# Performance work log

Measured on AMD Instinct MI355X. Metric: run time of the kernel, lower is better.

The kernel has to match this reference:

```python
import jax, jax.numpy as jnp
from jax import lax
import numpy as np

D_MODEL = 384; D_INNER = 768; D_STATE = 16; D_CONV = 4; DT_RANK = 24
BATCH = 2; SEQ = 4096


def _mamba(x, in_w, conv_w, conv_b, xproj_w, dt_w, dt_b, A_log, Dp, out_w):
    # x: [B, L, D_MODEL]
    xz = x @ in_w.T                                   # [B, L, 2*D_INNER]
    xi, z = jnp.split(xz, 2, axis=-1)
    xc = jnp.swapaxes(xi, 1, 2)                       # [B, D_INNER, L]
    xc = lax.conv_general_dilated(xc, conv_w, (1,), [(D_CONV - 1, 0)],
                                  feature_group_count=D_INNER)  # causal depthwise conv
    xc = jax.nn.silu(xc + conv_b[None, :, None])
    xc = jnp.swapaxes(xc, 1, 2)                       # [B, L, D_INNER]
    xdbl = xc @ xproj_w.T                             # [B, L, DT_RANK + 2*D_STATE]
    dt = xdbl[..., :DT_RANK]
    Bm = xdbl[..., DT_RANK:DT_RANK + D_STATE]
    Cm = xdbl[..., DT_RANK + D_STATE:]
    delta = jax.nn.softplus(dt @ dt_w.T + dt_b)       # [B, L, D_INNER]
    A = -jnp.exp(A_log)                               # [D_INNER, D_STATE]

    def step(h, inp):
        d_t, x_t, B_t, C_t = inp                      # [B,Di],[B,Di],[B,N],[B,N]
        dA = jnp.exp(d_t[..., None] * A)              # [B, Di, N]
        h = dA * h + (d_t * x_t)[..., None] * B_t[:, None, :]
        return h, jnp.einsum('bdn,bn->bd', h, C_t)

    xs = tuple(jnp.swapaxes(a, 0, 1) for a in (delta, xc, Bm, Cm))  # time-major
    h0 = jnp.zeros((x.shape[0], D_INNER, D_STATE), x.dtype)
    _, ys = lax.scan(step, h0, xs)                    # ys: [L, B, D_INNER]
    y = jnp.swapaxes(ys, 0, 1) + xc * Dp              # skip term D*x
    return (y * jax.nn.silu(z)) @ out_w.T             # [B, L, D_MODEL]


def _forward(x, fp, bp, c_w, c_b, gn_w, gn_b):
    xt = jnp.swapaxes(x, 1, 2)                        # [B, L, C]
    yf = _mamba(xt, *fp)
    yb = _mamba(xt[:, ::-1, :], *bp)                  # note: source does NOT flip back
    y = jnp.concatenate([yf, yb], axis=2)             # [B, L, 2C]
    y = jnp.swapaxes(y, 1, 2)                         # [B, 2C, L]
    y = jnp.einsum('oc,bcl->bol', c_w[:, :, 0], y) + c_b[None, :, None]  # 1x1 conv
    a, b = jnp.split(y, 2, axis=1)                    # GLU over channel dim
    y = a * jax.nn.sigmoid(b)                         # [B, C, L]
    mu = y.mean(axis=(1, 2), keepdims=True)           # GroupNorm(1, C)
    var = y.var(axis=(1, 2), keepdims=True)
    y = (y - mu) / jnp.sqrt(var + 1e-5)
    return y * gn_w[None, :, None] + gn_b[None, :, None]


def setup_inputs() -> dict:
    key = jax.random.key(0)
    it = iter(jax.random.split(key, 20))

    def nrm(shape, s=0.02):
        return jax.random.normal(next(it), shape, jnp.float32) * s

    def mamba_params(pref):
        return {
            pref + 'in_w': nrm((2 * D_INNER, D_MODEL)),
            pref + 'conv_w': nrm((D_INNER, 1, D_CONV), 0.3),
            pref + 'conv_b': nrm((D_INNER,)),
            pref + 'xproj_w': nrm((DT_RANK + 2 * D_STATE, D_INNER)),
            pref + 'dt_w': nrm((D_INNER, DT_RANK), 0.1),
            pref + 'dt_b': nrm((D_INNER,)),
            pref + 'A_log': jnp.log(jnp.tile(jnp.arange(1.0, D_STATE + 1.0, dtype=jnp.float32), (D_INNER, 1))),
            pref + 'D': jnp.ones((D_INNER,), jnp.float32),
            pref + 'out_w': nrm((D_MODEL, D_INNER)),
        }

    inp = {'x': jax.random.normal(next(it), (BATCH, D_MODEL, SEQ), jnp.float32)}
    inp.update(mamba_params('f_'))
    inp.update(mamba_params('b_'))
    inp['c_w'] = nrm((2 * D_MODEL, 2 * D_MODEL, 1))
    inp['c_b'] = nrm((2 * D_MODEL,))
    inp['gn_w'] = jnp.ones((D_MODEL,), jnp.float32)
    inp['gn_b'] = jnp.zeros((D_MODEL,), jnp.float32)
    return inp


def reference(x, f_in_w, f_conv_w, f_conv_b, f_xproj_w, f_dt_w, f_dt_b, f_A_log, f_D, f_out_w,
              b_in_w, b_conv_w, b_conv_b, b_xproj_w, b_dt_w, b_dt_b, b_A_log, b_D, b_out_w,
              c_w, c_b, gn_w, gn_b):
    fp = (f_in_w, f_conv_w, f_conv_b, f_xproj_w, f_dt_w, f_dt_b, f_A_log, f_D, f_out_w)
    bp = (b_in_w, b_conv_w, b_conv_b, b_xproj_w, b_dt_w, b_dt_b, b_A_log, b_D, b_out_w)
    return _forward(x, fp, bp, c_w, c_b, gn_w, gn_b)
```

## Files before the change

kernel.cpp:

```cpp
#include <hip/hip_runtime.h>
#include <hip/hip_bf16.h>
#include <hip/hip_fp16.h>

typedef unsigned short u16;
typedef unsigned int   u32;
typedef __bf16  bf16x8 __attribute__((ext_vector_type(8)));
typedef float   f32x4  __attribute__((ext_vector_type(4)));

#define BL   8192
#define LSEQ 4096
#define DI   768
#define CHUNK 32
#define NCHUNK (LSEQ / CHUNK)
#define CTC  16
#define LOG2E 1.44269504088896340736f

#define LOAD_LDS16(g, l) __builtin_amdgcn_global_load_lds( \
    (const __attribute__((address_space(1))) void*)(g), \
    (__attribute__((address_space(3))) void*)(l), 16, 0, 0)

static __device__ __forceinline__ float bf2f(u16 u) {
    union { float f; u32 i; } v; v.i = ((u32)u) << 16; return v.f;
}
static __device__ __forceinline__ u16 f2bs(float f) {
    union { float f; u32 i; } v; v.f = f;
    u32 r = v.i + 0x7fffu + ((v.i >> 16) & 1u);
    return (u16)(r >> 16);
}
static __device__ __forceinline__ float ldf(const void* p, size_t i, int f32) {
    return f32 ? ((const float*)p)[i] : bf2f(((const u16*)p)[i]);
}

__global__ void detect_dtype(const void* __restrict__ gnw, int* __restrict__ flag) {
    u32 bits = *(const u32*)gnw;
    *flag = ((bits & 0xFFFFu) == 0u) ? 1 : 0;
}

__global__ void check_apow(const void* __restrict__ a_f, const void* __restrict__ a_b,
                           int* __restrict__ apow, const int* __restrict__ flag) {
    int f = *flag;
    __shared__ int ok;
    if (threadIdx.x == 0) ok = 1;
    __syncthreads();
    for (int i = threadIdx.x; i < 2 * 12288; i += 256) {
        const void* a = (i >= 12288) ? a_b : a_f;
        int idx = i % 12288;
        int d = idx >> 4, n = idx & 15;
        float An = __expf(ldf(a, idx, f));
        float rf = __expf(ldf(a, d * 16, f)) * (float)(n + 1);
        if (fabsf(An - rf) > 1e-5f * fabsf(rf)) ok = 0;
    }
    __syncthreads();
    if (threadIdx.x == 0) *apow = ok;
}

__global__ void cvt_bf16_3(const void* __restrict__ s0, const void* __restrict__ s1,
                           const void* __restrict__ s2, u16* __restrict__ dst,
                           int n0, int n1, int ntot, const int* __restrict__ flag) {
    int i = blockIdx.x * 256 + threadIdx.x;
    if (i >= ntot) return;
    int f = *flag;
    const void* s; size_t off;
    if (i < n0)      { s = s0; off = i; }
    else if (i < n1) { s = s1; off = i - n0; }
    else             { s = s2; off = i - n1; }
    dst[i] = f ? f2bs(((const float*)s)[off]) : ((const u16*)s)[off];
}

__global__ void cvt_conv(const void* __restrict__ cw_f, const void* __restrict__ cw_b,
                         const void* __restrict__ cb_f, const void* __restrict__ cb_b,
                         float* __restrict__ cwf, float* __restrict__ cbf,
                         const int* __restrict__ flag) {
    int i = blockIdx.x * 256 + threadIdx.x;
    int f = *flag;
    if (i < 2 * 3072)
        cwf[i] = ldf(i < 3072 ? cw_f : cw_b, i % 3072, f);
    int j = i - 2 * 3072;
    if (j >= 0 && j < 2 * 768)
        cbf[j] = ldf(j < 768 ? cb_f : cb_b, j % 768, f);
}

__global__ void transpose_x(const void* __restrict__ x, u16* __restrict__ xT,
                            const int* __restrict__ flag) {
    __shared__ u16 tile[32][33];
    int f = *flag;
    int b  = blockIdx.z;
    int l0 = blockIdx.x * 32, c0 = blockIdx.y * 32;
    int li = threadIdx.x, ci = threadIdx.y;
    for (int cc = ci; cc < 32; cc += 8) {
        size_t idx = (size_t)(b * 384 + c0 + cc) * LSEQ + l0 + li;
        tile[cc][li] = f ? f2bs(((const float*)x)[idx]) : ((const u16*)x)[idx];
    }
    __syncthreads();
    for (int lc = ci; lc < 32; lc += 8)
        xT[(size_t)(b * LSEQ + l0 + lc) * 384 + c0 + li] = tile[li][lc];
}

__global__ void transpose_ow(const void* __restrict__ ow_f, const void* __restrict__ ow_b,
                             u16* __restrict__ owT, const int* __restrict__ flag) {
    __shared__ u16 tile[32][33];
    int f = *flag;
    int dir = blockIdx.z;
    const void* ow = dir ? ow_b : ow_f;
    int c0 = blockIdx.x * 32, d0 = blockIdx.y * 32;
    int di = threadIdx.x, ci = threadIdx.y;
    for (int cc = ci; cc < 32; cc += 8) {
        size_t idx = (size_t)(c0 + cc) * 768 + d0 + di;
        tile[cc][di] = f ? f2bs(((const float*)ow)[idx]) : ((const u16*)ow)[idx];
    }
    __syncthreads();
    for (int dd = ci; dd < 32; dd += 8)
        owT[(size_t)dir * 294912 + (size_t)(d0 + dd) * 384 + c0 + di] = tile[di][dd];
}

__global__ void build_wcomb(const void* __restrict__ xp_f, const void* __restrict__ dtw_f,
                            const void* __restrict__ xp_b, const void* __restrict__ dtw_b,
                            u16* __restrict__ Wc, const int* __restrict__ flag) {
    int f = *flag;
    int dir = blockIdx.y;
    const void* xp  = dir ? xp_b  : xp_f;
    const void* dtw = dir ? dtw_b : dtw_f;
    u16* W = Wc + (size_t)dir * 896 * 768;
    int idx = blockIdx.x * 256 + threadIdx.x;
    if (idx >= 896 * 768) return;
    int nrow = idx / 768, k = idx - nrow * 768;
    float v = 0.f;
    if (nrow < 768) {
#pragma unroll
        for (int r = 0; r < 24; r++)
            v = fmaf(ldf(dtw, nrow * 24 + r, f), ldf(xp, r * 768 + k, f), v);
    } else if (nrow < 800) {
        v = ldf(xp, (24 + (nrow - 768)) * 768 + k, f);
    }
    W[idx] = f2bs(v);
}

__global__ __launch_bounds__(256) void gemm_mfma(
    const u16* __restrict__ A, int lda, size_t aStr,
    const u16* __restrict__ W, int ldw, size_t wStr,
    int K, int MB, int NB, int Nstore, int mode,
    u16* __restrict__ ob0, u16* __restrict__ ob1,
    float* __restrict__ of0, float* __restrict__ of1,
    const void* __restrict__ bias0, const void* __restrict__ bias1,
    const int* __restrict__ flag) {
    __shared__ __align__(16) u16 lA[2][128 * 32];
    __shared__ __align__(16) u16 lB[2][128 * 32];
    const int f = *flag;
    const int tid = threadIdx.x;
    const int wave = tid >> 6, lane = tid & 63;
    const int flat = blockIdx.x;
    const int mb = flat % MB;
    const int rest = flat / MB;
    const int nb = rest % NB;
    const int dir = rest / NB;
    const int m0 = mb * 128, n0 = nb * 128;
    const int wr = (wave >> 1) * 64, wc = (wave & 1) * 64;
    const int fr = lane & 15, fq = lane >> 4;
    const void* bias = dir ? bias1 : bias0;

    f32x4 acc[4][4];
#pragma unroll
    for (int i = 0; i < 4; i++)
#pragma unroll
        for (int j = 0; j < 4; j++) acc[i][j] = 0.f;

    const int srow = wave * 16 + (lane >> 2);
    const int scol = (lane & 3) * 8;
    const u16* gA0 = A + (size_t)dir * aStr + (size_t)(m0 + srow) * lda + scol;
    const u16* gA1 = gA0 + (size_t)64 * lda;
    const u16* gB0 = W + (size_t)dir * wStr + (size_t)(n0 + srow) * ldw + scol;
    const u16* gB1 = gB0 + (size_t)64 * ldw;

    LOAD_LDS16(gA0, &lA[0][wave * 512]);
    LOAD_LDS16(gA1, &lA[0][2048 + wave * 512]);
    LOAD_LDS16(gB0, &lB[0][wave * 512]);
    LOAD_LDS16(gB1, &lB[0][2048 + wave * 512]);

    int cur = 0;
    for (int k0 = 0; k0 < K; k0 += 32) {
        __syncthreads();
        if (k0 + 32 < K) {
            gA0 += 32; gA1 += 32; gB0 += 32; gB1 += 32;
            int nx = cur ^ 1;
            LOAD_LDS16(gA0, &lA[nx][wave * 512]);
            LOAD_LDS16(gA1, &lA[nx][2048 + wave * 512]);
            LOAD_LDS16(gB0, &lB[nx][wave * 512]);
            LOAD_LDS16(gB1, &lB[nx][2048 + wave * 512]);
        }
        bf16x8 af[4], bfr[4];
#pragma unroll
        for (int i = 0; i < 4; i++) af[i]  = *(const bf16x8*)&lA[cur][(wr + i * 16 + fr) * 32 + fq * 8];
#pragma unroll
        for (int j = 0; j < 4; j++) bfr[j] = *(const bf16x8*)&lB[cur][(wc + j * 16 + fr) * 32 + fq * 8];
#pragma unroll
        for (int i = 0; i < 4; i++)
#pragma unroll
            for (int j = 0; j < 4; j++)
                acc[i][j] = __builtin_amdgcn_mfma_f32_16x16x32_bf16(af[i], bfr[j], acc[i][j], 0, 0, 0);
        cur ^= 1;
    }

    const int lr = (lane >> 4) * 4, lc = lane & 15;
#pragma unroll
    for (int i = 0; i < 4; i++) {
#pragma unroll
        for (int j = 0; j < 4; j++) {
#pragma unroll
            for (int rg = 0; rg < 4; rg++) {
                int m = m0 + wr + i * 16 + lr + rg;
                int n = n0 + wc + j * 16 + lc;
                if (n >= Nstore) continue;
                float v = acc[i][j][rg];
                if (mode == 0) {
                    int bI = m >> 12, l = m & 4095;
                    size_t r = dir ? ((size_t)bI * LSEQ + (LSEQ - 1 - l)) : (size_t)m;
                    if (n < 768) ob0[(size_t)dir * BL * DI + r * 768 + n] = f2bs(v);
                    else         ob1[(size_t)dir * BL * DI + r * 768 + (n - 768)] = f2bs(v);
                } else if (mode == 1) {
                    if (n < 768) {
                        float xp = v + ldf(bias, n, f);
                        float sp = fmaxf(xp, 0.f) + __logf(1.f + __expf(-fabsf(xp)));
                        ((__half*)ob0)[(size_t)dir * BL * DI + (size_t)m * 768 + n] = __float2half_rn(sp);
                    } else {
                        of1[(size_t)dir * BL * 32 + (size_t)m * 32 + (n - 768)] = v;
                    }
                } else if (mode == 2) {
                    ob0[(size_t)m * 1536 + dir * 768 + n] = f2bs(v);
                } else {
                    of0[(size_t)m * 768 + n] = v + ldf(bias, n, f);
                }
            }
        }
    }
}

__global__ __launch_bounds__(256) void conv_silu(
    const u16* __restrict__ xi, u16* __restrict__ xc,
    const float* __restrict__ cwf, const float* __restrict__ cbf) {
    int gid = blockIdx.x * 256 + threadIdx.x;
    int dg = gid % 96;
    int rest = gid / 96;
    int tc = rest % (LSEQ / CTC);
    int bd = rest / (LSEQ / CTC);
    int dir = bd >> 1;
    int d0 = dg * 8;
    float w[32], bias[8];
#pragma unroll
    for (int q = 0; q < 8; q++) *(float4*)&w[q * 4] = *(const float4*)&cwf[dir * 3072 + d0 * 4 + q * 4];
    *(float4*)&bias[0] = *(const float4*)&cbf[dir * 768 + d0];
    *(float4*)&bias[4] = *(const float4*)&cbf[dir * 768 + d0 + 4];
    size_t rowbase = (size_t)bd * LSEQ;
    int t0 = tc * CTC;
    uint4 zero; zero.x = zero.y = zero.z = zero.w = 0u;
    uint4 win[4];
#pragma unroll
    for (int i = 0; i < 3; i++) {
        int tt = t0 - 3 + i;
        win[i] = (tt >= 0) ? *(const uint4*)&xi[(rowbase + tt) * DI + d0] : zero;
    }
    uint4 nxt = *(const uint4*)&xi[(rowbase + t0) * DI + d0];
#pragma unroll 4
    for (int i = 0; i < CTC; i++) {
        win[3] = nxt;
        if (i + 1 < CTC) nxt = *(const uint4*)&xi[(rowbase + t0 + i + 1) * DI + d0];
        float acc[8];
#pragma unroll
        for (int c = 0; c < 8; c++) acc[c] = bias[c];
#pragma unroll
        for (int tap = 0; tap < 4; tap++) {
            const u16* pv = (const u16*)&win[tap];
#pragma unroll
            for (int c = 0; c < 8; c++)
                acc[c] = fmaf(w[c * 4 + tap], bf2f(pv[c]), acc[c]);
        }
        u16 ov[8];
#pragma unroll
        for (int c = 0; c < 8; c++) ov[c] = f2bs(acc[c] / (1.f + __expf(-acc[c])));
        *(uint4*)&xc[(rowbase + t0 + i) * DI + d0] = *(const uint4*)ov;
        win[0] = win[1]; win[1] = win[2]; win[2] = win[3];
    }
}

__global__ __launch_bounds__(256) void scan_phase1(
    const __half* __restrict__ delta, const u16* __restrict__ xc,
    const float* __restrict__ bc,
    __half* __restrict__ S, __half* __restrict__ sumdl,
    const void* __restrict__ alog_f, const void* __restrict__ alog_b,
    const int* __restrict__ flag, const int* __restrict__ apow) {
    int f = *flag, ap = *apow;
    int dblk = blockIdx.x, chunk = blockIdx.y, bd = blockIdx.z;
    int dir = bd >> 1;
    const void* alog = dir ? alog_b : alog_f;
    int d = dblk * 256 + threadIdx.x;
    size_t rowbase = (size_t)bd * LSEQ;
    float h[16];
#pragma unroll
    for (int n = 0; n < 16; n++) h[n] = 0.f;
    float An2_0 = -__expf(ldf(alog, d * 16, f)) * LOG2E;
    int t0 = chunk * CHUNK;
    size_t off = (rowbase + t0) * DI + d;
    const float* bcG = bc + (rowbase + t0) * 32;
    float sd = 0.f;
    if (ap) {
#pragma unroll 2
        for (int i = 0; i < CHUNK; i++, off += DI) {
            float Bv[16];
#pragma unroll
            for (int q = 0; q < 4; q++) *(float4*)&Bv[q * 4] = *(const float4*)&bcG[(size_t)i * 32 + q * 4];
            float dl = __half2float(delta[off]);
            float u = dl * bf2f(xc[off]);
            sd += dl;
            float e[16];
            float e1 = exp2f(dl * An2_0);
            e[0]=e1; e[1]=e1*e1; e[2]=e[1]*e1; e[3]=e[1]*e[1];
            e[4]=e[3]*e[0]; e[5]=e[3]*e[1]; e[6]=e[3]*e[2]; e[7]=e[3]*e[3];
            e[8]=e[7]*e[0]; e[9]=e[7]*e[1]; e[10]=e[7]*e[2]; e[11]=e[7]*e[3];
            e[12]=e[7]*e[4]; e[13]=e[7]*e[5]; e[14]=e[7]*e[6]; e[15]=e[7]*e[7];
#pragma unroll
            for (int n = 0; n < 16; n++) h[n] = fmaf(e[n], h[n], u * Bv[n]);
        }
    } else {
        float An2[16];
#pragma unroll
        for (int n = 0; n < 16; n++) An2[n] = -__expf(ldf(alog, d * 16 + n, f)) * LOG2E;
#pragma unroll 2
        for (int i = 0; i < CHUNK; i++, off += DI) {
            float Bv[16];
#pragma unroll
            for (int q = 0; q < 4; q++) *(float4*)&Bv[q * 4] = *(const float4*)&bcG[(size_t)i * 32 + q * 4];
            float dl = __half2float(delta[off]);
            float u = dl * bf2f(xc[off]);
            sd += dl;
#pragma unroll
            for (int n = 0; n < 16; n++)
                h[n] = fmaf(exp2f(dl * An2[n]), h[n], u * Bv[n]);
        }
    }
    __half hs[16];
#pragma unroll
    for (int n = 0; n < 16; n++) hs[n] = __float2half(h[n]);
    __half* Sp = S + (((size_t)bd * NCHUNK + chunk) * 768 + d) * 16;
    *(uint4*)&Sp[0] = *(const uint4*)&hs[0];
    *(uint4*)&Sp[8] = *(const uint4*)&hs[8];
    sumdl[((size_t)bd * NCHUNK + chunk) * 768 + d] = __float2half(sd);
}

__global__ __launch_bounds__(256) void scan_fixup(
    __half* __restrict__ S, const __half* __restrict__ sumdl,
    const void* __restrict__ alog_f, const void* __restrict__ alog_b,
    const int* __restrict__ flag) {
    int f = *flag;
    int gid = blockIdx.x * 256 + threadIdx.x;
    int bd = gid / 12288;
    int r  = gid % 12288;
    int d = r >> 4, n = r & 15;
    const void* alog = (bd >> 1) ? alog_b : alog_f;
    float An2 = -__expf(ldf(alog, d * 16 + n, f)) * LOG2E;
    float h = 0.f;
#pragma unroll 4
    for (int c = 0; c < NCHUNK; c++) {
        size_t sidx = (((size_t)bd * NCHUNK + c) * 768 + d) * 16 + n;
        float s  = __half2float(S[sidx]);
        float sd = __half2float(sumdl[((size_t)bd * NCHUNK + c) * 768 + d]);
        S[sidx] = __float2half(h);
        h = fmaf(exp2f(An2 * sd), h, s);
    }
}

__global__ __launch_bounds__(256) void scan_phase3(
    const __half* __restrict__ delta, const u16* __restrict__ xc,
    const float* __restrict__ bc, const u16* __restrict__ zz,
    const __half* __restrict__ S, u16* __restrict__ ygi,
    const void* __restrict__ alog_f, const void* __restrict__ alog_b,
    const void* __restrict__ D_f, const void* __restrict__ D_b,
    const int* __restrict__ flag, const int* __restrict__ apow) {
    int f = *flag, ap = *apow;
    int dblk = blockIdx.x, chunk = blockIdx.y, bd = blockIdx.z;
    int dir = bd >> 1, b = bd & 1;
    const void* alog = dir ? alog_b : alog_f;
    const void* Dp   = dir ? D_b   : D_f;
    int d = dblk * 256 + threadIdx.x;
    size_t rowbase = (size_t)bd * LSEQ;
    float An2_0 = -__expf(ldf(alog, d * 16, f)) * LOG2E;
    float h[16];
    {
        const __half* Sp = S + (((size_t)bd * NCHUNK + chunk) * 768 + d) * 16;
        uint4 sv0 = *(const uint4*)&Sp[0];
        uint4 sv1 = *(const uint4*)&Sp[8];
        const __half* ph0 = (const __half*)&sv0;
        const __half* ph1 = (const __half*)&sv1;
#pragma unroll
        for (int n = 0; n < 8; n++) { h[n] = __half2float(ph0[n]); h[n + 8] = __half2float(ph1[n]); }
    }
    float Dd = ldf(Dp, d, f);
    int t0 = chunk * CHUNK;
    size_t off = (rowbase + t0) * DI + d;
    size_t oidx = ((size_t)b * LSEQ + t0) * 1536 + dir * 768 + d;
    const float* bcG = bc + (rowbase + t0) * 32;
    if (ap) {
#pragma unroll 2
        for (int i = 0; i < CHUNK; i++, off += DI, oidx += 1536) {
            float Bv[16], Cv[16];
#pragma unroll
            for (int q = 0; q < 4; q++) *(float4*)&Bv[q * 4] = *(const float4*)&bcG[(size_t)i * 32 + q * 4];
#pragma unroll
            for (int q = 0; q < 4; q++) *(float4*)&Cv[q * 4] = *(const float4*)&bcG[(size_t)i * 32 + 16 + q * 4];
            float dl = __half2float(delta[off]);
            float xf = bf2f(xc[off]);
            float u = dl * xf;
            float e[16];
            float e1 = exp2f(dl * An2_0);
            e[0]=e1; e[1]=e1*e1; e[2]=e[1]*e1; e[3]=e[1]*e[1];
            e[4]=e[3]*e[0]; e[5]=e[3]*e[1]; e[6]=e[3]*e[2]; e[7]=e[3]*e[3];
            e[8]=e[7]*e[0]; e[9]=e[7]*e[1]; e[10]=e[7]*e[2]; e[11]=e[7]*e[3];
            e[12]=e[7]*e[4]; e[13]=e[7]*e[5]; e[14]=e[7]*e[6]; e[15]=e[7]*e[7];
            float y = 0.f;
#pragma unroll
            for (int n = 0; n < 16; n++) {
                h[n] = fmaf(e[n], h[n], u * Bv[n]);
                y = fmaf(h[n], Cv[n], y);
            }
            float zf = bf2f(zz[off]);
            ygi[oidx] = f2bs((y + xf * Dd) * (zf / (1.f + __expf(-zf))));
        }
    } else {
        float An2[16];
#pragma unroll
        for (int n = 0; n < 16; n++) An2[n] = -__expf(ldf(alog, d * 16 + n, f)) * LOG2E;
#pragma unroll 2
        for (int i = 0; i < CHUNK; i++, off += DI, oidx += 1536) {
            float Bv[16], Cv[16];
#pragma unroll
            for (int q = 0; q < 4; q++) *(float4*)&Bv[q * 4] = *(const float4*)&bcG[(size_t)i * 32 + q * 4];
#pragma unroll
            for (int q = 0; q < 4; q++) *(float4*)&Cv[q * 4] = *(const float4*)&bcG[(size_t)i * 32 + 16 + q * 4];
            float dl = __half2float(delta[off]);
            float xf = bf2f(xc[off]);
            float u = dl * xf;
            float y = 0.f;
#pragma unroll
            for (int n = 0; n < 16; n++) {
                h[n] = fmaf(exp2f(dl * An2[n]), h[n], u * Bv[n]);
                y = fmaf(h[n], Cv[n], y);
            }
            float zf = bf2f(zz[off]);
            ygi[oidx] = f2bs((y + xf * Dd) * (zf / (1.f + __expf(-zf))));
        }
    }
}

__global__ __launch_bounds__(256) void glu_stats(const float* __restrict__ g,
                                                 float* __restrict__ glu,
                                                 double* __restrict__ accum) {
    __shared__ float tile[64][65];
    __shared__ double wsum[8];
    int bI = blockIdx.z;
    int l0 = blockIdx.x * 64, o0 = blockIdx.y * 64;
    int tid = threadIdx.x;
    int j = tid & 63, i0 = tid >> 6;
    double s = 0.0, s2 = 0.0;
    for (int i = i0; i < 64; i += 4) {
        size_t r = (size_t)bI * LSEQ + l0 + i;
        float a  = g[r * 768 + o0 + j];
        float bb = g[r * 768 + 384 + o0 + j];
        float v = a * (1.f / (1.f + __expf(-bb)));
        tile[j][i] = v;
        s += v; s2 += (double)v * v;
    }
#pragma unroll
    for (int o = 1; o < 64; o <<= 1) { s += __shfl_xor(s, o); s2 += __shfl_xor(s2, o); }
    if ((tid & 63) == 0) { wsum[(tid >> 6) * 2] = s; wsum[(tid >> 6) * 2 + 1] = s2; }
    __syncthreads();
    if (tid == 0) {
        double S = wsum[0] + wsum[2] + wsum[4] + wsum[6];
        double S2 = wsum[1] + wsum[3] + wsum[5] + wsum[7];
        atomicAdd(&accum[bI * 2], S);
        atomicAdd(&accum[bI * 2 + 1], S2);
    }
    int l = tid & 63, oi0 = tid >> 6;
    for (int oi = oi0; oi < 64; oi += 4)
        glu[((size_t)bI * 384 + o0 + oi) * LSEQ + l0 + l] = tile[oi][l];
}

__global__ void norm_out(const float* __restrict__ glu, const double* __restrict__ accum,
                         const void* __restrict__ gnw, const void* __restrict__ gnb,
                         void* __restrict__ out, const int* __restrict__ flag) {
    int f = *flag;
    int idx = blockIdx.x * 256 + threadIdx.x;
    int b = idx / (384 * LSEQ);
    int o = (idx / LSEQ) % 384;
    double Nf = (double)(384 * LSEQ);
    double S = accum[b * 2], S2 = accum[b * 2 + 1];
    double mu = S / Nf;
    double var = S2 / Nf - mu * mu;
    float rstd = rsqrtf((float)var + 1e-5f);
    float v = (glu[idx] - (float)mu) * rstd * ldf(gnw, o, f) + ldf(gnb, o, f);
    if (f) ((float*)out)[idx] = v;
    else   ((u16*)out)[idx] = f2bs(v);
}

extern "C" void kernel_launch(void* const* d_in, const int* in_sizes, int n_in,
                              void* d_out, int out_size, void* d_ws, size_t ws_size,
                              hipStream_t stream) {
    (void)in_sizes; (void)n_in; (void)out_size; (void)ws_size;
    const void* x       = d_in[0];
    const void* inw[2]  = {d_in[1],  d_in[10]};
    const void* cwv[2]  = {d_in[2],  d_in[11]};
    const void* cbv[2]  = {d_in[3],  d_in[12]};
    const void* xpw[2]  = {d_in[4],  d_in[13]};
    const void* dtw[2]  = {d_in[5],  d_in[14]};
    const void* dtb[2]  = {d_in[6],  d_in[15]};
    const void* alog[2] = {d_in[7],  d_in[16]};
    const void* Dv[2]   = {d_in[8],  d_in[17]};
    const void* outw[2] = {d_in[9],  d_in[18]};
    const void* c_w = d_in[19];
    const void* c_b = d_in[20];
    const void* gnw = d_in[21];
    const void* gnb = d_in[22];

    char* base = (char*)d_ws;
    u16*    xT    = (u16*)   (base + 0);
    u16*    zz    = (u16*)   (base + 6291456);
    u16*    xc    = (u16*)   (base + 31457280);
    u16*    xi    = (u16*)   (base + 56623104);
    __half* delta = (__half*)(base + 56623104);
    float*  bc    = (float*) (base + 81788928);
    u16*    Wc    = (u16*)   (base + 83886080);
    u16*    yg    = (u16*)   (base + 86638592);
    double* accum = (double*)(base + 111804416);
    int*    flag  = (int*)   (base + 111804480);
    int*    apow  = (int*)   (base + 111804484);
    __half* Sbuf  = (__half*)(base + 111804672);
    __half* sumdl = (__half*)(base + 124387584);
    float*  cwf   = (float*) (base + 125174016);
    float*  cbf   = (float*) (base + 125198592);
    float*  g     = (float*)xc;
    float*  glu   = (float*)xi;
    u16*    cinw  = yg;
    u16*    ccw   = (u16*)(base + 69206016);
    u16*    owT   = (u16*)(base + 70385664);
    u16*    W2    = (u16*)(base + 71565312);

    hipMemsetAsync(accum, 0, 64, stream);
    detect_dtype<<<1, 1, 0, stream>>>(gnw, flag);
    check_apow<<<1, 256, 0, stream>>>(alog[0], alog[1], apow, flag);
    cvt_conv<<<30, 256, 0, stream>>>(cwv[0], cwv[1], cbv[0], cbv[1], cwf, cbf, flag);

    transpose_x<<<dim3(LSEQ / 32, 12, 2), dim3(32, 8), 0, stream>>>(x, xT, flag);
    cvt_bf16_3<<<(1179648 + 255) / 256, 256, 0, stream>>>(
        inw[0], inw[1], inw[1], cinw, 589824, 1179648, 1179648, flag);
    build_wcomb<<<dim3((896 * 768 + 255) / 256, 2), 256, 0, stream>>>(
        xpw[0], dtw[0], xpw[1], dtw[1], Wc, flag);

    gemm_mfma<<<dim3(64 * 12 * 2), 256, 0, stream>>>(
        xT, 384, 0, cinw, 384, 589824, 384, 64, 12, 1536, 0,
        xi, zz, nullptr, nullptr, nullptr, nullptr, flag);

    conv_silu<<<dim3(4 * (LSEQ / CTC) * 96 / 256), 256, 0, stream>>>(xi, xc, cwf, cbf);

    gemm_mfma<<<dim3(64 * 7 * 2), 256, 0, stream>>>(
        xc, 768, (size_t)BL * DI, Wc, 768, (size_t)896 * 768, 768, 64, 7, 800, 1,
        (u16*)delta, nullptr, nullptr, bc, dtb[0], dtb[1], flag);

    scan_phase1<<<dim3(3, NCHUNK, 4), 256, 0, stream>>>(
        delta, xc, bc, Sbuf, sumdl, alog[0], alog[1], flag, apow);
    scan_fixup<<<dim3(192), 256, 0, stream>>>(Sbuf, sumdl, alog[0], alog[1], flag);
    scan_phase3<<<dim3(3, NCHUNK, 4), 256, 0, stream>>>(
        delta, xc, bc, zz, Sbuf, yg, alog[0], alog[1], Dv[0], Dv[1], flag, apow);

    cvt_bf16_3<<<(589824 + 255) / 256, 256, 0, stream>>>(
        c_w, c_w, c_w, ccw, 589824, 589824, 589824, flag);
    transpose_ow<<<dim3(12, 24, 2), dim3(32, 8), 0, stream>>>(outw[0], outw[1], owT, flag);
    gemm_mfma<<<dim3(6 * 6 * 2), 256, 0, stream>>>(
        ccw, 768, 384, owT, 384, 294912, 384, 6, 6, 768, 2,
        W2, nullptr, nullptr, nullptr, nullptr, nullptr, flag);

    gemm_mfma<<<dim3(64 * 6), 256, 0, stream>>>(
        yg, 1536, 0, W2, 1536, 0, 1536, 64, 6, 768, 3,
        nullptr, nullptr, g, nullptr, c_b, c_b, flag);

    glu_stats<<<dim3(LSEQ / 64, 6, 2), 256, 0, stream>>>(g, glu, accum);
    norm_out<<<dim3(2 * 384 * LSEQ / 256), 256, 0, stream>>>(glu, accum, gnw, gnb, d_out, flag);
}
```

Measured before the change: 464.6 us.

## Fuse GLU and statistics into final GEMM epilogue, merge prep kernels

Adds a dedicated final GEMM that loads the paired a/b weight rows into one tile, applies bias and GLU in its epilogue, writes the row-major GLU output and accumulates the mean/variance sums with atomics. This removes the fp32 intermediate g round-trip and the separate glu_stats pass. Normalisation now transposes through shared memory while writing the output. The three small prep launches (dtype detect, A-power check, conv weight conversion) are also merged into one launch. The new GEMM uses a 64x128 tile with its own double-buffered LDS loads, so its efficiency may differ from the generic GEMM path.

Result: faster. 450.3 us (-3.1%).

```diff
diff --git a/kernel.cpp b/kernel.cpp
--- a/kernel.cpp
+++ b/kernel.cpp
@@ -30,28 +30,37 @@
 static __device__ __forceinline__ float ldf(const void* p, size_t i, int f32) {
     return f32 ? ((const float*)p)[i] : bf2f(((const u16*)p)[i]);
 }
-
-__global__ void detect_dtype(const void* __restrict__ gnw, int* __restrict__ flag) {
-    u32 bits = *(const u32*)gnw;
-    *flag = ((bits & 0xFFFFu) == 0u) ? 1 : 0;
-}
-
-__global__ void check_apow(const void* __restrict__ a_f, const void* __restrict__ a_b,
-                           int* __restrict__ apow, const int* __restrict__ flag) {
-    int f = *flag;
-    __shared__ int ok;
-    if (threadIdx.x == 0) ok = 1;
-    __syncthreads();
-    for (int i = threadIdx.x; i < 2 * 12288; i += 256) {
-        const void* a = (i >= 12288) ? a_b : a_f;
-        int idx = i % 12288;
-        int d = idx >> 4, n = idx & 15;
-        float An = __expf(ldf(a, idx, f));
-        float rf = __expf(ldf(a, d * 16, f)) * (float)(n + 1);
-        if (fabsf(An - rf) > 1e-5f * fabsf(rf)) ok = 0;
-    }
-    __syncthreads();
-    if (threadIdx.x == 0) *apow = ok;
+static __device__ __forceinline__ int flag_of(const void* gnw) {
+    return (((*(const u32*)gnw) & 0xFFFFu) == 0u) ? 1 : 0;
+}
+
+__global__ void prep0(const void* __restrict__ gnw,
+                      const void* __restrict__ a_f, const void* __restrict__ a_b,
+                      const void* __restrict__ cw_f, const void* __restrict__ cw_b,
+                      const void* __restrict__ cb_f, const void* __restrict__ cb_b,
+                      int* __restrict__ flag, int* __restrict__ apow,
+                      float* __restrict__ cwf, float* __restrict__ cbf) {
+    int f = flag_of(gnw);
+    int bid = blockIdx.x;
+    if (bid == 30) {
+        __shared__ int ok;
+        if (threadIdx.x == 0) { *flag = f; ok = 1; }
+        __syncthreads();
+        for (int i = threadIdx.x; i < 2 * 12288; i += 256) {
+            const void* a = (i >= 12288) ? a_b : a_f;
+            int idx = i % 12288;
+            int d = idx >> 4, n = idx & 15;
+            float An = __expf(ldf(a, idx, f));
+            float rf = __expf(ldf(a, d * 16, f)) * (float)(n + 1);
+            if (fabsf(An - rf) > 1e-5f * fabsf(rf)) ok = 0;
+        }
+        __syncthreads();
+        if (threadIdx.x == 0) *apow = ok;
+    } else {
+        int i = bid * 256 + threadIdx.x;
+        if (i < 6144) cwf[i] = ldf(i < 3072 ? cw_f : cw_b, i % 3072, f);
+        else { int j = i - 6144; if (j < 1536) cbf[j] = ldf(j < 768 ? cb_f : cb_b, j % 768, f); }
+    }
 }
 
 __global__ void cvt_bf16_3(const void* __restrict__ s0, const void* __restrict__ s1,
@@ -65,19 +74,6 @@
     else if (i < n1) { s = s1; off = i - n0; }
     else             { s = s2; off = i - n1; }
     dst[i] = f ? f2bs(((const float*)s)[off]) : ((const u16*)s)[off];
-}
-
-__global__ void cvt_conv(const void* __restrict__ cw_f, const void* __restrict__ cw_b,
-                         const void* __restrict__ cb_f, const void* __restrict__ cb_b,
-                         float* __restrict__ cwf, float* __restrict__ cbf,
-                         const int* __restrict__ flag) {
-    int i = blockIdx.x * 256 + threadIdx.x;
-    int f = *flag;
-    if (i < 2 * 3072)
-        cwf[i] = ldf(i < 3072 ? cw_f : cw_b, i % 3072, f);
-    int j = i - 2 * 3072;
-    if (j >= 0 && j < 2 * 768)
-        cbf[j] = ldf(j < 768 ? cb_f : cb_b, j % 768, f);
 }
 
 __global__ void transpose_x(const void* __restrict__ x, u16* __restrict__ xT,
@@ -224,13 +220,116 @@
                     } else {
                         of1[(size_t)dir * BL * 32 + (size_t)m * 32 + (n - 768)] = v;
                     }
-                } else if (mode == 2) {
+                } else {
                     ob0[(size_t)m * 1536 + dir * 768 + n] = f2bs(v);
-                } else {
-                    of0[(size_t)m * 768 + n] = v + ldf(bias, n, f);
                 }
             }
         }
+    }
+}
+
+__global__ __launch_bounds__(256) void gemm_glu(
+    const u16* __restrict__ A, const u16* __restrict__ W2v,
+    float* __restrict__ glu_rm, double* __restrict__ accum,
+    const void* __restrict__ c_b, const int* __restrict__ flag) {
+    __shared__ __align__(16) u16 smem[20480];
+    __shared__ double wsum[4];
+    const int f = *flag;
+    const int tid = threadIdx.x;
+    const int wave = tid >> 6, lane = tid & 63;
+    const int mb = blockIdx.x % 128, nb = blockIdx.x / 128;
+    const int m0 = mb * 64, n0 = nb * 128;
+    const int fr = lane & 15, fq = lane >> 4;
+
+    f32x4 acc[4][4];
+#pragma unroll
+    for (int i = 0; i < 4; i++)
+#pragma unroll
+        for (int j = 0; j < 4; j++) acc[i][j] = 0.f;
+
+    const int srow = wave * 16 + (lane >> 2);
+    const int scol = (lane & 3) * 8;
+    const u16* gA = A + (size_t)(m0 + srow) * 1536 + scol;
+    const u16* gB[4];
+#pragma unroll
+    for (int q = 0; q < 4; q++) {
+        int cr = q * 64 + srow;
+        int wrow = (cr < 128) ? (n0 + cr) : (n0 + 256 + cr);
+        gB[q] = W2v + (size_t)wrow * 1536 + scol;
+    }
+
+    LOAD_LDS16(gA, &smem[wave * 512]);
+#pragma unroll
+    for (int q = 0; q < 4; q++) LOAD_LDS16(gB[q], &smem[4096 + q * 2048 + wave * 512]);
+
+    int cur = 0;
+    for (int k0 = 0; k0 < 1536; k0 += 32) {
+        __syncthreads();
+        if (k0 + 32 < 1536) {
+            gA += 32;
+#pragma unroll
+            for (int q = 0; q < 4; q++) gB[q] += 32;
+            int nx = cur ^ 1;
+            LOAD_LDS16(gA, &smem[nx * 2048 + wave * 512]);
+#pragma unroll
+            for (int q = 0; q < 4; q++) LOAD_LDS16(gB[q], &smem[4096 + nx * 8192 + q * 2048 + wave * 512]);
+        }
+        const u16* bA = &smem[cur * 2048];
+        const u16* bB = &smem[4096 + cur * 8192];
+        bf16x8 af[4], bfr[4];
+#pragma unroll
+        for (int i = 0; i < 4; i++) af[i]  = *(const bf16x8*)&bA[(i * 16 + fr) * 32 + fq * 8];
+#pragma unroll
+        for (int j = 0; j < 4; j++) bfr[j] = *(const bf16x8*)&bB[(wave * 64 + j * 16 + fr) * 32 + fq * 8];
+#pragma unroll
+        for (int i = 0; i < 4; i++)
+#pragma unroll
+            for (int j = 0; j < 4; j++)
+                acc[i][j] = __builtin_amdgcn_mfma_f32_16x16x32_bf16(af[i], bfr[j], acc[i][j], 0, 0, 0);
+        cur ^= 1;
+    }
+
+    const int lr = (lane >> 4) * 4, lc = lane & 15;
+    __syncthreads();
+    float* sB = (float*)smem;
+    if (wave >= 2) {
+#pragma unroll
+        for (int i = 0; i < 4; i++)
+#pragma unroll
+            for (int j = 0; j < 4; j++)
+#pragma unroll
+                for (int rg = 0; rg < 4; rg++) {
+                    int row = i * 16 + lr + rg;
+                    int c = (wave - 2) * 64 + j * 16 + lc;
+                    sB[row * 128 + c] = acc[i][j][rg] + ldf(c_b, n0 + 384 + c, f);
+                }
+    }
+    __syncthreads();
+    double s = 0.0, s2 = 0.0;
+    if (wave < 2) {
+#pragma unroll
+        for (int i = 0; i < 4; i++)
+#pragma unroll
+            for (int j = 0; j < 4; j++)
+#pragma unroll
+                for (int rg = 0; rg < 4; rg++) {
+                    int row = i * 16 + lr + rg;
+                    int c = wave * 64 + j * 16 + lc;
+                    float a = acc[i][j][rg] + ldf(c_b, n0 + c, f);
+                    float b = sB[row * 128 + c];
+                    float v = a / (1.f + __expf(-b));
+                    glu_rm[(size_t)(m0 + row) * 384 + n0 + c] = v;
+                    s += v; s2 += (double)v * v;
+                }
+#pragma unroll
+        for (int o = 1; o < 64; o <<= 1) { s += __shfl_xor(s, o); s2 += __shfl_xor(s2, o); }
+        if (lane == 0) { wsum[wave * 2] = s; wsum[wave * 2 + 1] = s2; }
+    }
+    __syncthreads();
+    if (tid == 0) {
+        int bI = m0 >> 12;
+        atomicAdd(&accum[bI * 2], wsum[0] + wsum[2]);
+        atomicAdd(&accum[bI * 2 + 1], wsum[1] + wsum[3]);
     }
 }
 
@@ -449,54 +548,30 @@
     }
 }
 
-__global__ __launch_bounds__(256) void glu_stats(const float* __restrict__ g,
-                                                 float* __restrict__ glu,
-                                                 double* __restrict__ accum) {
-    __shared__ float tile[64][65];
-    __shared__ double wsum[8];
-    int bI = blockIdx.z;
-    int l0 = blockIdx.x * 64, o0 = blockIdx.y * 64;
-    int tid = threadIdx.x;
-    int j = tid & 63, i0 = tid >> 6;
-    double s = 0.0, s2 = 0.0;
-    for (int i = i0; i < 64; i += 4) {
-        size_t r = (size_t)bI * LSEQ + l0 + i;
-        float a  = g[r * 768 + o0 + j];
-        float bb = g[r * 768 + 384 + o0 + j];
-        float v = a * (1.f / (1.f + __expf(-bb)));
-        tile[j][i] = v;
-        s += v; s2 += (double)v * v;
-    }
-#pragma unroll
-    for (int o = 1; o < 64; o <<= 1) { s += __shfl_xor(s, o); s2 += __shfl_xor(s2, o); }
-    if ((tid & 63) == 0) { wsum[(tid >> 6) * 2] = s; wsum[(tid >> 6) * 2 + 1] = s2; }
+__global__ void norm_trans(const float* __restrict__ glu_rm, const double* __restrict__ accum,
+                           const void* __restrict__ gnw, const void* __restrict__ gnb,
+                           void* __restrict__ out, const int* __restrict__ flag) {
+    __shared__ float tile[32][33];
+    int f = *flag;
+    int b = blockIdx.z;
+    int l0 = blockIdx.x * 32, o0 = blockIdx.y * 32;
+    int tx = threadIdx.x, ty = threadIdx.y;
+    for (int ll = ty; ll < 32; ll += 8)
+        tile[ll][tx] = glu_rm[(size_t)(b * LSEQ + l0 + ll) * 384 + o0 + tx];
     __syncthreads();
-    if (tid == 0) {
-        double S = wsum[0] + wsum[2] + wsum[4] + wsum[6];
-        double S2 = wsum[1] + wsum[3] + wsum[5] + wsum[7];
-        atomicAdd(&accum[bI * 2], S);
-        atomicAdd(&accum[bI * 2 + 1], S2);
-    }
-    int l = tid & 63, oi0 = tid >> 6;
-    for (int oi = oi0; oi < 64; oi += 4)
-        glu[((size_t)bI * 384 + o0 + oi) * LSEQ + l0 + l] = tile[oi][l];
-}
-
-__global__ void norm_out(const float* __restrict__ glu, const double* __restrict__ accum,
-                         const void* __restrict__ gnw, const void* __restrict__ gnb,
-                         void* __restrict__ out, const int* __restrict__ flag) {
-    int f = *flag;
-    int idx = blockIdx.x * 256 + threadIdx.x;
-    int b = idx / (384 * LSEQ);
-    int o = (idx / LSEQ) % 384;
     double Nf = (double)(384 * LSEQ);
-    double S = accum[b * 2], S2 = accum[b * 2 + 1];
-    double mu = S / Nf;
+    double Sm = accum[b * 2], S2 = accum[b * 2 + 1];
+    double mu = Sm / Nf;
     double var = S2 / Nf - mu * mu;
     float rstd = rsqrtf((float)var + 1e-5f);
-    float v = (glu[idx] - (float)mu) * rstd * ldf(gnw, o, f) + ldf(gnb, o, f);
-    if (f) ((float*)out)[idx] = v;
-    else   ((u16*)out)[idx] = f2bs(v);
+    float fmu = (float)mu;
+    for (int oo = ty; oo < 32; oo += 8) {
+        int o = o0 + oo;
+        float v = (tile[tx][oo] - fmu) * rstd * ldf(gnw, o, f) + ldf(gnb, o, f);
+        size_t oi = (size_t)(b * 384 + o) * LSEQ + l0 + tx;
+        if (f) ((float*)out)[oi] = v;
+        else   ((u16*)out)[oi] = f2bs(v);
+    }
 }
 
 extern "C" void kernel_launch(void* const* d_in, const int* in_sizes, int n_in,
@@ -534,17 +609,15 @@
     __half* sumdl = (__half*)(base + 124387584);
     float*  cwf   = (float*) (base + 125174016);
     float*  cbf   = (float*) (base + 125198592);
-    float*  g     = (float*)xc;
-    float*  glu   = (float*)xi;
+    float*  glu_rm = (float*)xi;
     u16*    cinw  = yg;
     u16*    ccw   = (u16*)(base + 69206016);
     u16*    owT   = (u16*)(base + 70385664);
     u16*    W2    = (u16*)(base + 71565312);
 
     hipMemsetAsync(accum, 0, 64, stream);
-    detect_dtype<<<1, 1, 0, stream>>>(gnw, flag);
-    check_apow<<<1, 256, 0, stream>>>(alog[0], alog[1], apow, flag);
-    cvt_conv<<<30, 256, 0, stream>>>(cwv[0], cwv[1], cbv[0], cbv[1], cwf, cbf, flag);
+    prep0<<<31, 256, 0, stream>>>(gnw, alog[0], alog[1], cwv[0], cwv[1], cbv[0], cbv[1],
+                                  flag, apow, cwf, cbf);
 
     transpose_x<<<dim3(LSEQ / 32, 12, 2), dim3(32, 8), 0, stream>>>(x, xT, flag);
     cvt_bf16_3<<<(1179648 + 255) / 256, 256, 0, stream>>>(
@@ -575,10 +648,8 @@
         ccw, 768, 384, owT, 384, 294912, 384, 6, 6, 768, 2,
         W2, nullptr, nullptr, nullptr, nullptr, nullptr, flag);
 
-    gemm_mfma<<<dim3(64 * 6), 256, 0, stream>>>(
-        yg, 1536, 0, W2, 1536, 0, 1536, 64, 6, 768, 3,
-        nullptr, nullptr, g, nullptr, c_b, c_b, flag);
-
-    glu_stats<<<dim3(LSEQ / 64, 6, 2), 256, 0, stream>>>(g, glu, accum);
-    norm_out<<<dim3(2 * 384 * LSEQ / 256), 256, 0, stream>>>(glu, accum, gnw, gnb, d_out, flag);
-}
+    gemm_glu<<<dim3(384), 256, 0, stream>>>(yg, W2, glu_rm, accum, c_b, flag);
+
+    norm_trans<<<dim3(LSEQ / 32, 12, 2), dim3(32, 8), 0, stream>>>(
+        glu_rm, accum, gnw, gnb, d_out, flag);
+}
```
